# Optimization experiments

Hardware: AMD Instinct MI355X
Metric: run time of the kernel (lower is better)

Reference implementation:

```python
import jax, jax.numpy as jnp
import numpy as np

# Static config mirroring init_kwargs
N, C, H, W = 2, 10, 30, 30
PAD = 4                    # pad_size
HL = WL = 1 + 2 * PAD      # 9x9 local window
MAXH = MAXW = 10           # max_height / max_width
L = MAXH * MAXW            # tokens per pixel sequence = 100
D = C + 1                  # d_model = 11 (color channels + pad indicator)
EPS = 1e-5


def setup_inputs() -> dict:
    key = jax.random.key(0)
    ks = jax.random.split(key, 7)
    # one-hot ARC-style grid: each pixel is one of C colors
    classes = jax.random.randint(ks[0], (N, H, W), 0, C)
    x = jax.nn.one_hot(classes, C, dtype=jnp.float32).transpose(0, 3, 1, 2)  # [N,C,H,W]
    s = 0.1
    w_in = jax.random.normal(ks[1], (3 * D, D), dtype=jnp.float32) * s   # in_proj_weight
    w_out = jax.random.normal(ks[2], (D, D), dtype=jnp.float32) * s     # out_proj
    w_ff1 = jax.random.normal(ks[3], (1, D), dtype=jnp.float32) * s     # linear1 (D->1)
    w_ff2 = jax.random.normal(ks[4], (D, 1), dtype=jnp.float32) * s     # linear2 (1->D)
    ln1_g = jnp.ones((D,), dtype=jnp.float32)
    ln2_g = jnp.ones((D,), dtype=jnp.float32)
    return {"x": x, "w_in": w_in, "w_out": w_out, "w_ff1": w_ff1,
            "w_ff2": w_ff2, "ln1_g": ln1_g, "ln2_g": ln2_g}


def _layernorm(x, g):
    m = jnp.mean(x, axis=-1, keepdims=True)
    v = jnp.var(x, axis=-1, keepdims=True)
    return (x - m) / jnp.sqrt(v + EPS) * g


def reference(x, w_in, w_out, w_ff1, w_ff2, ln1_g, ln2_g):
    # pad colors with pad_value=0, pad-indicator channel with 1 in the border
    xp = jnp.pad(x, ((0, 0), (0, 0), (PAD, PAD), (PAD, PAD)))
    ind = jnp.pad(jnp.zeros((N, 1, H, W), x.dtype),
                  ((0, 0), (0, 0), (PAD, PAD), (PAD, PAD)), constant_values=1.0)
    xa = jnp.concatenate([xp, ind], axis=1).transpose(0, 2, 3, 1)  # [N,Hp,Wp,D]

    # im2col: 9x9 window around every pixel
    ii = jnp.arange(H)[:, None] + jnp.arange(HL)[None, :]  # [H,HL]
    jj = jnp.arange(W)[:, None] + jnp.arange(WL)[None, :]  # [W,WL]
    patches = xa[:, ii[:, None, :, None], jj[None, :, None, :], :]   # [N,H,W,HL,WL,D]
    patches = patches.transpose(0, 1, 2, 5, 3, 4)                    # [N,H,W,D,HL,WL]
    # embed window into max_height x max_width canvas (fill = pad_value = 0)
    patches = jnp.pad(patches, ((0, 0),) * 4 + ((0, MAXH - HL), (0, MAXW - WL)))
    seq = patches.reshape(N * H * W, D, L).transpose(0, 2, 1)        # [B,L,D]

    mask_inf = jnp.all(seq == 0, axis=2)               # [B,L] key padding mask
    mask0 = (seq[:, :, -1:] == 1).astype(seq.dtype)    # [B,L,1] border-padding gate

    # --- TransformerEncoderLayer (post-norm, bias=False, eval/no-dropout) ---
    qkv = seq @ w_in.T                                 # [B,L,3D]
    q, k, v = jnp.split(qkv, 3, axis=-1)
    # nhead = D, head_dim = 1, scale = 1/sqrt(1) = 1 -> per-channel outer products
    scores = jnp.einsum('bqd,bkd->bdqk', q, k)         # [B,D,L,L]
    scores = jnp.where(mask_inf[:, None, None, :], -1e9, scores)
    attn = jax.nn.softmax(scores, axis=-1)
    ao = jnp.einsum('bdqk,bkd->bqd', attn, v) @ w_out.T
    h = _layernorm(seq + ao, ln1_g)
    ff = jax.nn.relu(h @ w_ff1.T) @ w_ff2.T            # D -> 1 -> D
    h = _layernorm(h + ff, ln2_g)

    # softmax over color channels, zero out everywhere except padded border tokens
    colored = jax.nn.softmax(h[:, :, :-1], axis=2) * mask0
    out = (seq[:, :, :-1] + colored).transpose(0, 2, 1)  # [B,C,L]
    return out
```

## Files before the change

kernel.cpp:

```cpp
#include <hip/hip_runtime.h>

#define NB   2
#define CC   10
#define HH   30
#define WW   30
#define PADR 4
#define DD   11
#define NPIX (NB*HH*WW)

__global__ __launch_bounds__(128) void pve_fused(
    const float* __restrict__ x,
    const float* __restrict__ w_in,
    const float* __restrict__ w_out,
    const float* __restrict__ w_ff1,
    const float* __restrict__ w_ff2,
    const float* __restrict__ ln1g,
    const float* __restrict__ ln2g,
    float* __restrict__ out)
{
    __shared__ float E[121];
    __shared__ float EV[121];
    __shared__ float WO[121];
    __shared__ float G1[11], G2[11], F1[11], F2[11];
    __shared__ int   cnt[11];
    __shared__ float smvS[10];
    __shared__ unsigned char chs[100];

    const int t = threadIdx.x;
    const int pix = blockIdx.x;
    const int n  = pix / (HH * WW);
    const int rm = pix % (HH * WW);
    const int i0 = rm / WW, j0 = rm % WW;

    if (t < 121) {
        const int d = t / 11, c = t % 11;
        const float Q = w_in[d * DD + 10];
        const float K = w_in[(DD + d) * DD + c];
        const float V = w_in[(2 * DD + d) * DD + c];
        const float e = __expf(Q * K);
        E[t] = e; EV[t] = e * V; WO[t] = w_out[t];
    }
    if (t < 11) {
        G1[t] = ln1g[t]; G2[t] = ln2g[t];
        F1[t] = w_ff1[t]; F2[t] = w_ff2[t];
        cnt[t] = 0;
    }
    __syncthreads();

    if (t < 100) {
        const int ph = t / 10, pw = t % 10;
        unsigned int c = 255;
        if (ph < 9 && pw < 9) {
            const int r  = i0 + ph - PADR;
            const int cc = j0 + pw - PADR;
            c = 10;
            if (r >= 0 && r < HH && cc >= 0 && cc < WW) {
                const float* xp = x + n * CC * HH * WW + r * WW + cc;
                int cls = 10;
                #pragma unroll
                for (int k = CC - 1; k >= 0; k--) {
                    if (xp[k * HH * WW] > 0.5f) cls = k;
                }
                c = (unsigned int)cls;
            }
            atomicAdd(&cnt[c], 1);
        }
        chs[t] = (unsigned char)c;
    }
    __syncthreads();

    if (t < 16) {
        const int g = t;
        const int d = (g < 11) ? g : 0;

        float s1 = 0.f, s2 = 0.f;
        #pragma unroll
        for (int c = 0; c < 11; c++) {
            const float cn = (float)cnt[c];
            s1 += cn * E[d * 11 + c];
            s2 += cn * EV[d * 11 + c];
        }
        const float ao = s2 / s1;

        float h = 0.f;
        #pragma unroll
        for (int j = 0; j < 11; j++)
            h += WO[d * 11 + j] * __shfl(ao, j, 16);
        if (g == 10) h += 1.0f;
        if (g >= 11) h = 0.f;

        float s = h;
        #pragma unroll
        for (int m = 1; m < 16; m <<= 1) s += __shfl_xor(s, m, 16);
        float mean = s * (1.f / 11.f);
        float dv = (g < 11) ? (h - mean) : 0.f;
        float sq = dv * dv;
        #pragma unroll
        for (int m = 1; m < 16; m <<= 1) sq += __shfl_xor(sq, m, 16);
        const float hb = dv * rsqrtf(sq * (1.f / 11.f) + 1e-5f) * G1[d];

        float f = hb * F1[d];
        #pragma unroll
        for (int m = 1; m < 16; m <<= 1) f += __shfl_xor(f, m, 16);
        f = fmaxf(f, 0.f);
        float h2 = hb + f * F2[d];
        if (g >= 11) h2 = 0.f;

        s = h2;
        #pragma unroll
        for (int m = 1; m < 16; m <<= 1) s += __shfl_xor(s, m, 16);
        mean = s * (1.f / 11.f);
        dv = (g < 11) ? (h2 - mean) : 0.f;
        sq = dv * dv;
        #pragma unroll
        for (int m = 1; m < 16; m <<= 1) sq += __shfl_xor(sq, m, 16);
        const float hc = dv * rsqrtf(sq * (1.f / 11.f) + 1e-5f) * G2[d];

        float mv = (g < 10) ? hc : -1e30f;
        #pragma unroll
        for (int m = 1; m < 16; m <<= 1) mv = fmaxf(mv, __shfl_xor(mv, m, 16));
        const float ex = (g < 10) ? __expf(hc - mv) : 0.f;
        float den = ex;
        #pragma unroll
        for (int m = 1; m < 16; m <<= 1) den += __shfl_xor(den, m, 16);
        if (g < 10) smvS[g] = ex / den;
    }
    __syncthreads();

    float* po = out + (size_t)pix * 1000;
    #pragma unroll
    for (int it = 0; it < 2; it++) {
        const int vi = t + it * 128;
        if (vi < 250) {
            const int idx = vi * 4;
            const int c   = idx / 100;
            const int l0  = idx - c * 100;
            const uchar4 c4 = *reinterpret_cast<const uchar4*>(chs + l0);
            const float sv = smvS[c];
            float4 v4;
            v4.x = (c4.x == 255) ? 0.f : ((c4.x < 10) ? ((c == c4.x) ? 1.f : 0.f) : sv);
            v4.y = (c4.y == 255) ? 0.f : ((c4.y < 10) ? ((c == c4.y) ? 1.f : 0.f) : sv);
            v4.z = (c4.z == 255) ? 0.f : ((c4.z < 10) ? ((c == c4.z) ? 1.f : 0.f) : sv);
            v4.w = (c4.w == 255) ? 0.f : ((c4.w < 10) ? ((c == c4.w) ? 1.f : 0.f) : sv);
            reinterpret_cast<float4*>(po)[vi] = v4;
        }
    }
}

extern "C" void kernel_launch(void* const* d_in, const int* in_sizes, int n_in,
                              void* d_out, int out_size, void* d_ws, size_t ws_size,
                              hipStream_t stream) {
    const float* x     = (const float*)d_in[0];
    const float* w_in  = (const float*)d_in[1];
    const float* w_out = (const float*)d_in[2];
    const float* w_ff1 = (const float*)d_in[3];
    const float* w_ff2 = (const float*)d_in[4];
    const float* ln1g  = (const float*)d_in[5];
    const float* ln2g  = (const float*)d_in[6];
    float* out = (float*)d_out;

    pve_fused<<<NPIX, 128, 0, stream>>>(x, w_in, w_out, w_ff1, w_ff2,
                                        ln1g, ln2g, out);
}
```

Baseline: 73.61 us.

## Replace shared atomics with packed warp-shuffle histogram, use 256-thread blocks

Window classification now runs on a separate 64-lane wavefront (threads 128-191), which concurrently with the weight-table setup builds the class histogram. Counts are packed as bytes in three registers and reduced with shuffles, which removes the shared-memory atomics and one block barrier. The block grows to 256 threads so the output write needs one pass. The ao broadcast is moved from a width-16 shuffle to a volatile shared array. The larger block adds idle threads, and each lane now classifies up to two positions, which lengthens the serial critical path.

After: 73.03 us. No clear change (-0.8%).

```diff
diff --git a/kernel.cpp b/kernel.cpp
--- a/kernel.cpp
+++ b/kernel.cpp
@@ -8,7 +8,7 @@
 #define DD   11
 #define NPIX (NB*HH*WW)
 
-__global__ __launch_bounds__(128) void pve_fused(
+__global__ __launch_bounds__(256) void pve_fused(
     const float* __restrict__ x,
     const float* __restrict__ w_in,
     const float* __restrict__ w_out,
@@ -22,8 +22,9 @@
     __shared__ float EV[121];
     __shared__ float WO[121];
     __shared__ float G1[11], G2[11], F1[11], F2[11];
-    __shared__ int   cnt[11];
+    __shared__ float cntf[11];
     __shared__ float smvS[10];
+    volatile __shared__ float aoS[16];
     __shared__ unsigned char chs[100];
 
     const int t = threadIdx.x;
@@ -43,29 +44,42 @@
     if (t < 11) {
         G1[t] = ln1g[t]; G2[t] = ln2g[t];
         F1[t] = w_ff1[t]; F2[t] = w_ff2[t];
-        cnt[t] = 0;
     }
-    __syncthreads();
 
-    if (t < 100) {
-        const int ph = t / 10, pw = t % 10;
-        unsigned int c = 255;
-        if (ph < 9 && pw < 9) {
-            const int r  = i0 + ph - PADR;
-            const int cc = j0 + pw - PADR;
-            c = 10;
-            if (r >= 0 && r < HH && cc >= 0 && cc < WW) {
-                const float* xp = x + n * CC * HH * WW + r * WW + cc;
-                int cls = 10;
-                #pragma unroll
-                for (int k = CC - 1; k >= 0; k--) {
-                    if (xp[k * HH * WW] > 0.5f) cls = k;
+    if (t >= 128 && t < 192) {
+        const int lane = t - 128;
+        unsigned int pk0 = 0, pk1 = 0, pk2 = 0;
+        for (int l = lane; l < 100; l += 64) {
+            const int ph = l / 10, pw = l % 10;
+            unsigned int c = 255;
+            if (ph < 9 && pw < 9) {
+                const int r  = i0 + ph - PADR;
+                const int cc = j0 + pw - PADR;
+                c = 10;
+                if (r >= 0 && r < HH && cc >= 0 && cc < WW) {
+                    const float* xp = x + n * CC * HH * WW + r * WW + cc;
+                    int cls = 10;
+                    #pragma unroll
+                    for (int k = CC - 1; k >= 0; k--) {
+                        if (xp[k * HH * WW] > 0.5f) cls = k;
+                    }
+                    c = (unsigned int)cls;
                 }
-                c = (unsigned int)cls;
+                const unsigned int inc = 1u << ((c & 3) * 8);
+                if (c < 4) pk0 += inc; else if (c < 8) pk1 += inc; else pk2 += inc;
             }
-            atomicAdd(&cnt[c], 1);
+            chs[l] = (unsigned char)c;
         }
-        chs[t] = (unsigned char)c;
+        #pragma unroll
+        for (int m = 1; m < 64; m <<= 1) {
+            pk0 += __shfl_xor(pk0, m, 64);
+            pk1 += __shfl_xor(pk1, m, 64);
+            pk2 += __shfl_xor(pk2, m, 64);
+        }
+        if (lane < 11) {
+            const unsigned int pk = (lane < 4) ? pk0 : ((lane < 8) ? pk1 : pk2);
+            cntf[lane] = (float)((pk >> ((lane & 3) * 8)) & 0xFFu);
+        }
     }
     __syncthreads();
 
@@ -76,16 +90,17 @@
         float s1 = 0.f, s2 = 0.f;
         #pragma unroll
         for (int c = 0; c < 11; c++) {
-            const float cn = (float)cnt[c];
+            const float cn = cntf[c];
             s1 += cn * E[d * 11 + c];
             s2 += cn * EV[d * 11 + c];
         }
         const float ao = s2 / s1;
 
+        aoS[g] = ao;
         float h = 0.f;
         #pragma unroll
         for (int j = 0; j < 11; j++)
-            h += WO[d * 11 + j] * __shfl(ao, j, 16);
+            h += WO[d * 11 + j] * aoS[j];
         if (g == 10) h += 1.0f;
         if (g >= 11) h = 0.f;
 
@@ -127,23 +142,18 @@
     }
     __syncthreads();
 
-    float* po = out + (size_t)pix * 1000;
-    #pragma unroll
-    for (int it = 0; it < 2; it++) {
-        const int vi = t + it * 128;
-        if (vi < 250) {
-            const int idx = vi * 4;
-            const int c   = idx / 100;
-            const int l0  = idx - c * 100;
-            const uchar4 c4 = *reinterpret_cast<const uchar4*>(chs + l0);
-            const float sv = smvS[c];
-            float4 v4;
-            v4.x = (c4.x == 255) ? 0.f : ((c4.x < 10) ? ((c == c4.x) ? 1.f : 0.f) : sv);
-            v4.y = (c4.y == 255) ? 0.f : ((c4.y < 10) ? ((c == c4.y) ? 1.f : 0.f) : sv);
-            v4.z = (c4.z == 255) ? 0.f : ((c4.z < 10) ? ((c == c4.z) ? 1.f : 0.f) : sv);
-            v4.w = (c4.w == 255) ? 0.f : ((c4.w < 10) ? ((c == c4.w) ? 1.f : 0.f) : sv);
-            reinterpret_cast<float4*>(po)[vi] = v4;
-        }
+    if (t < 250) {
+        const int idx = t * 4;
+        const int c   = idx / 100;
+        const int l0  = idx - c * 100;
+        const uchar4 c4 = *reinterpret_cast<const uchar4*>(chs + l0);
+        const float sv = smvS[c];
+        float4 v4;
+        v4.x = (c4.x == 255) ? 0.f : ((c4.x < 10) ? ((c == c4.x) ? 1.f : 0.f) : sv);
+        v4.y = (c4.y == 255) ? 0.f : ((c4.y < 10) ? ((c == c4.y) ? 1.f : 0.f) : sv);
+        v4.z = (c4.z == 255) ? 0.f : ((c4.z < 10) ? ((c == c4.z) ? 1.f : 0.f) : sv);
+        v4.w = (c4.w == 255) ? 0.f : ((c4.w < 10) ? ((c == c4.w) ? 1.f : 0.f) : sv);
+        reinterpret_cast<float4*>(out + (size_t)pix * 1000)[t] = v4;
     }
 }
 
@@ -159,6 +169,6 @@
     const float* ln2g  = (const float*)d_in[6];
     float* out = (float*)d_out;
 
-    pve_fused<<<NPIX, 128, 0, stream>>>(x, w_in, w_out, w_ff1, w_ff2,
+    pve_fused<<<NPIX, 256, 0, stream>>>(x, w_in, w_out, w_ff1, w_ff2,
                                         ln1g, ln2g, out);
 }
```
